# Kernel tuning notes

Hardware: AMD Instinct MI355X
Metric: run time of the kernel (lower is better)

The kernel has to match this reference:

```python
import jax, jax.numpy as jnp
import numpy as np

B, S, H = 1, 2048, 512
E = 16           # num_experts
K = 2            # num_experts_per_tok (norm_topk_prob=False -> no renorm)
I = 4 * H        # routed expert intermediate (mlp_ratio * embed_dim)
IS = 2 * H       # shared expert intermediate (embed_dim * n_shared_experts)


def setup_inputs() -> dict:
    key = jax.random.key(0)
    ks = jax.random.split(key, 9)
    scale = 1.0 / np.sqrt(H)
    return {
        "hidden_states": jax.random.normal(ks[0], (B, S, H), dtype=jnp.float32),
        "gate_w": jax.random.uniform(ks[1], (E, H), jnp.float32, -scale, scale),
        # routed experts, torch Linear weight layout [out, in]
        "w_gate": jax.random.uniform(ks[2], (E, I, H), jnp.float32, -scale, scale),
        "w_up": jax.random.uniform(ks[3], (E, I, H), jnp.float32, -scale, scale),
        "w_down": jax.random.uniform(ks[4], (E, H, I), jnp.float32, -1.0 / np.sqrt(I), 1.0 / np.sqrt(I)),
        # shared expert
        "sw_gate": jax.random.uniform(ks[5], (IS, H), jnp.float32, -scale, scale),
        "sw_up": jax.random.uniform(ks[6], (IS, H), jnp.float32, -scale, scale),
        "sw_down": jax.random.uniform(ks[7], (H, IS), jnp.float32, -1.0 / np.sqrt(IS), 1.0 / np.sqrt(IS)),
    }


def reference(hidden_states, gate_w, w_gate, w_up, w_down, sw_gate, sw_up, sw_down):
    b, s, h = hidden_states.shape
    x = hidden_states.reshape(-1, h)                       # [T, H]
    T = x.shape[0]

    # --- MoEGate: softmax scores, top-k (unnormalized weights) ---
    logits = jnp.einsum("th,eh->te", x, gate_w)            # [T, E]
    scores = jax.nn.softmax(logits, axis=-1)
    topk_w, topk_idx = jax.lax.top_k(scores, K)            # [T, K]

    # combine weights per (token, expert): zero unless selected
    combine = jnp.zeros((T, E), dtype=x.dtype).at[
        jnp.arange(T)[:, None], topk_idx
    ].add(topk_w)                                          # [T, E]

    # --- routed experts (SwiGLU), weighted scatter-combine ---
    g = jnp.einsum("th,eih->tei", x, w_gate)               # [T, E, I]
    u = jnp.einsum("th,eih->tei", x, w_up)
    inter = jax.nn.silu(g) * u                             # [T, E, I]
    y = jnp.einsum("tei,ehi,te->th", inter, w_down, combine)  # [T, H]

    # --- shared expert (always-on SwiGLU) ---
    sg = jax.nn.silu(x @ sw_gate.T) * (x @ sw_up.T)        # [T, IS]
    y = y + sg @ sw_down.T

    return y.reshape(b, s, h)
```

## Files before the change

kernel.cpp:

```cpp
#include <hip/hip_runtime.h>
#include <hip/hip_bf16.h>
#include <math.h>

#define T_TOK 2048
#define H_DIM 512
#define E_NUM 16
#define TOPK  2
#define I_DIM 2048
#define IS_DIM 1024
#define RPMAX 6144
#define NRT128 (RPMAX / 128)
#define NRT64  (RPMAX / 64)

typedef __attribute__((ext_vector_type(8))) short bf16x8;
typedef __attribute__((ext_vector_type(4))) float f32x4;
typedef unsigned short ushort_t;

static __device__ __forceinline__ unsigned short f2bf(float f) {
  unsigned int u = __float_as_uint(f);
  unsigned int r = (u + 0x7fffu + ((u >> 16) & 1u)) >> 16;
  return (unsigned short)r;
}

static __device__ __forceinline__ bf16x8 pack8(float4 a, float4 b) {
  bf16x8 v;
  v[0] = (short)f2bf(a.x); v[1] = (short)f2bf(a.y);
  v[2] = (short)f2bf(a.z); v[3] = (short)f2bf(a.w);
  v[4] = (short)f2bf(b.x); v[5] = (short)f2bf(b.y);
  v[6] = (short)f2bf(b.z); v[7] = (short)f2bf(b.w);
  return v;
}

static __device__ __forceinline__ unsigned long long cvt4(float4 v) {
  __hip_bfloat162 lo = __float22bfloat162_rn(make_float2(v.x, v.y));
  __hip_bfloat162 hi = __float22bfloat162_rn(make_float2(v.z, v.w));
  unsigned int ulo = *(unsigned int*)&lo;
  unsigned int uhi = *(unsigned int*)&hi;
  return ((unsigned long long)uhi << 32) | ulo;
}


template <int LKC>
__global__ __launch_bounds__(256) void gatherA_kernel(const float* __restrict__ x,
                                                      const int* __restrict__ row_token,
                                                      ushort_t* __restrict__ d,
                                                      int n8, int K) {
  const int KC = 1 << LKC;
  int i = blockIdx.x * 256 + threadIdx.x;
  int stride = gridDim.x * 256;
  for (; i < n8; i += stride) {
    int l  = i & 63;
    int fi = i >> 6;
    int kk = fi & (KC - 1);
    int rg = fi >> LKC;
    int row = rg * 16 + (l & 15);
    int tok = row_token ? row_token[row] : row;
    bf16x8 v = {};
    if (tok >= 0) {
      const float* p = x + (size_t)tok * K + kk * 32 + (l >> 4) * 8;
      v = pack8(*(const float4*)p, *(const float4*)(p + 4));
    }
    ((bf16x8*)d)[i] = v;
  }
}

__global__ __launch_bounds__(256) void logits_kernel(
    const float* __restrict__ x, const float* __restrict__ gw,
    float* __restrict__ logits)
{
  __shared__ float xs[16][516];
  int tid = threadIdx.x;
  int t0 = blockIdx.x * 16;
  for (int i = tid; i < 2048; i += 256) {
    int tt = i >> 7, q = i & 127;
    float4 v = ((const float4*)(x + (size_t)(t0 + tt) * H_DIM))[q];
    *(float4*)&xs[tt][q * 4] = v;
  }
  __syncthreads();
  int e = tid >> 4, tt = tid & 15;
  const float* gr = gw + (size_t)e * H_DIM;
  const float* xr = &xs[tt][0];
  int kbase = (blockIdx.x & 7) << 6;
  float acc = 0.f;
  #pragma unroll 8
  for (int kk = 0; kk < H_DIM; kk += 4) {
    int k = (kbase + kk) & (H_DIM - 1);
    float4 b = *(const float4*)(gr + k);
    float4 a = *(const float4*)(xr + k);
    acc += a.x * b.x + a.y * b.y + a.z * b.z + a.w * b.w;
  }
  logits[(size_t)(t0 + tt) * E_NUM + e] = acc;
}

__global__ __launch_bounds__(256) void topk_kernel(
    const float* __restrict__ logits,
    int* __restrict__ topk_idx, float* __restrict__ topk_w, int* __restrict__ counts)
{
  __shared__ int hist[E_NUM];
  int tid = threadIdx.x;
  if (tid < E_NUM) hist[tid] = 0;
  __syncthreads();
  int t = blockIdx.x * 256 + tid;
  float lg[E_NUM];
  #pragma unroll
  for (int i = 0; i < 4; i++) {
    float4 v = ((const float4*)(logits + (size_t)t * E_NUM))[i];
    lg[i * 4] = v.x; lg[i * 4 + 1] = v.y; lg[i * 4 + 2] = v.z; lg[i * 4 + 3] = v.w;
  }
  float mx = lg[0];
  #pragma unroll
  for (int i = 1; i < E_NUM; i++) mx = fmaxf(mx, lg[i]);
  float sc[E_NUM];
  float sum = 0.f;
  #pragma unroll
  for (int i = 0; i < E_NUM; i++) { sc[i] = expf(lg[i] - mx); sum += sc[i]; }
  float inv = 1.f / sum;
  float m1 = -1.f, m2 = -1.f; int i1 = 0, i2 = 0;
  #pragma unroll
  for (int i = 0; i < E_NUM; i++) {
    float s = sc[i] * inv;
    if (s > m1)      { m2 = m1; i2 = i1; m1 = s; i1 = i; }
    else if (s > m2) { m2 = s; i2 = i; }
  }
  topk_idx[t * 2] = i1; topk_idx[t * 2 + 1] = i2;
  topk_w[t * 2] = m1;  topk_w[t * 2 + 1] = m2;
  atomicAdd(&hist[i1], 1);
  atomicAdd(&hist[i2], 1);
  __syncthreads();
  if (tid < E_NUM) atomicAdd(&counts[tid], hist[tid]);
}

__global__ void offsets_kernel(const int* __restrict__ counts,
                               int* __restrict__ offp, int* __restrict__ cursor,
                               int* __restrict__ rt2e, int* __restrict__ rg2e)
{
  __shared__ int offs[E_NUM + 1];
  int tid = threadIdx.x;
  if (tid == 0) {
    int acc = 0;
    #pragma unroll
    for (int e = 0; e < E_NUM; e++) {
      offs[e] = acc; offp[e] = acc;
      acc += (counts[e] + 127) & ~127;
    }
    offs[E_NUM] = acc; offp[E_NUM] = acc;
  }
  if (tid < E_NUM) cursor[tid] = 0;
  __syncthreads();
  for (int r = tid; r < NRT128; r += 128) {
    int row = r << 7; int e = -1;
    #pragma unroll
    for (int i = 0; i < E_NUM; i++)
      if (row >= offs[i] && row < offs[i + 1]) e = i;
    rt2e[r] = e;
  }
  for (int r = tid; r < NRT64; r += 128) {
    int row = r << 6; int e = -1;
    #pragma unroll
    for (int i = 0; i < E_NUM; i++)
      if (row >= offs[i] && row < offs[i + 1]) e = i;
    rg2e[r] = e;
  }
}

__global__ __launch_bounds__(256) void initrows_kernel(int* __restrict__ row_token) {
  int i = blockIdx.x * 256 + threadIdx.x;
  if (i < RPMAX) row_token[i] = -1;
}

__global__ __launch_bounds__(256) void scatter_kernel(
    const int* __restrict__ topk_idx, const float* __restrict__ topk_w,
    const int* __restrict__ offp, int* __restrict__ cursor,
    int* __restrict__ row_token, int* __restrict__ trow)
{
  int t = blockIdx.x * 256 + threadIdx.x;
  if (t >= T_TOK) return;
  #pragma unroll
  for (int k = 0; k < TOPK; k++) {
    int e = topk_idx[t * 2 + k];
    int pos = atomicAdd(&cursor[e], 1);
    int row = offp[e] + pos;
    row_token[row] = t;
    trow[t * 2 + k] = row;
  }
}

__global__ __launch_bounds__(256, 2) void gu12_kernel(
    const ushort_t* __restrict__ xgf, const ushort_t* __restrict__ xsf,
    const float* __restrict__ wg_all, const float* __restrict__ wu_all,
    const float* __restrict__ swg, const float* __restrict__ swu,
    ushort_t* __restrict__ interF, ushort_t* __restrict__ interS,
    const int* __restrict__ rt2e)
{
  const int KC = H_DIM / 32;
  int bid = blockIdx.x;
  int tid = threadIdx.x, w = tid >> 6, l = tid & 63;
  int wm = w >> 1, wn = w & 1;
  int fr = l & 15, g = l >> 4;

  const bf16x8* AF; const float *WG, *WU;
  bf16x8* OP;
  int rg0, c0, kkd0, KCd;

  if (bid < 32 * NRT128) {
    int cb = bid & 31, rt = bid >> 5;
    int e = rt2e[rt]; if (e < 0) return;
    rg0 = rt * 8;
    AF = (const bf16x8*)xgf;
    WG = wg_all + (size_t)e * I_DIM * H_DIM;
    WU = wu_all + (size_t)e * I_DIM * H_DIM;
    c0 = cb * 64;
    KCd = I_DIM >> 5; kkd0 = cb * 2 + wn;
    OP = (bf16x8*)interF;
  } else {
    int b2 = bid - 32 * NRT128;
    int cb = b2 & 15, rt = b2 >> 4;
    rg0 = rt * 8;
    AF = (const bf16x8*)xsf;
    WG = swg; WU = swu;
    c0 = cb * 64;
    KCd = IS_DIM >> 5; kkd0 = cb * 2 + wn;
    OP = (bf16x8*)interS;
  }

  __shared__ ushort_t sm[2][8192];

  const bf16x8* abase[2]; int au[2];
  #pragma unroll
  for (int j = 0; j < 2; j++) {
    int u = tid + j * 256;
    au[j] = u;
    abase[j] = AF + ((size_t)(rg0 + (u >> 6)) * KC) * 64 + (u & 63);
  }
  const float* bgsrc[2]; int bws[2];
  #pragma unroll
  for (int i = 0; i < 2; i++) {
    int f = tid + i * 256;
    int row = f >> 3, q = f & 7;
    bgsrc[i] = WG + (size_t)(c0 + row) * H_DIM + q * 4;
    bws[i] = 8192 + (row >> 4) * 1024 + ((row & 15) + (q >> 1) * 16) * 16 + (q & 1) * 8;
  }
  ptrdiff_t dWU = WU - WG;

  f32x4 accg[4][2] = {}, accu[4][2] = {};
  bf16x8 ra0[2], ra1[2];
  float4 rg0v[2], ru0v[2], rg1v[2], ru1v[2];

  auto loadS0 = [&](int kk) {
    #pragma unroll
    for (int j = 0; j < 2; j++) ra0[j] = abase[j][(size_t)kk * 64];
    #pragma unroll
    for (int i = 0; i < 2; i++) {
      rg0v[i] = *(const float4*)(bgsrc[i] + kk * 32);
      ru0v[i] = *(const float4*)(bgsrc[i] + dWU + kk * 32);
    }
  };
  auto loadS1 = [&](int kk) {
    #pragma unroll
    for (int j = 0; j < 2; j++) ra1[j] = abase[j][(size_t)kk * 64];
    #pragma unroll
    for (int i = 0; i < 2; i++) {
      rg1v[i] = *(const float4*)(bgsrc[i] + kk * 32);
      ru1v[i] = *(const float4*)(bgsrc[i] + dWU + kk * 32);
    }
  };
  auto writeS0 = [&](int b) {
    bf16x8* ap = (bf16x8*)sm[b];
    ap[au[0]] = ra0[0]; ap[au[1]] = ra0[1];
    char* pb = (char*)sm[b];
    #pragma unroll
    for (int i = 0; i < 2; i++) {
      *(unsigned long long*)(pb + bws[i])        = cvt4(rg0v[i]);
      *(unsigned long long*)(pb + bws[i] + 4096) = cvt4(ru0v[i]);
    }
  };
  auto writeS1 = [&](int b) {
    bf16x8* ap = (bf16x8*)sm[b];
    ap[au[0]] = ra1[0]; ap[au[1]] = ra1[1];
    char* pb = (char*)sm[b];
    #pragma unroll
    for (int i = 0; i < 2; i++) {
      *(unsigned long long*)(pb + bws[i])        = cvt4(rg1v[i]);
      *(unsigned long long*)(pb + bws[i] + 4096) = cvt4(ru1v[i]);
    }
  };
  auto compute = [&](int b) {
    char* pb = (char*)sm[b];
    bf16x8 af[4], bg[2], bu[2];
    #pragma unroll
    for (int mi = 0; mi < 4; mi++)
      af[mi] = *(const bf16x8*)(pb + (wm * 4 + mi) * 1024 + l * 16);
    #pragma unroll
    for (int ni = 0; ni < 2; ni++) {
      bg[ni] = *(const bf16x8*)(pb + 8192  + (wn * 2 + ni) * 1024 + l * 16);
      bu[ni] = *(const bf16x8*)(pb + 12288 + (wn * 2 + ni) * 1024 + l * 16);
    }
    __builtin_amdgcn_s_setprio(1);
    #pragma unroll
    for (int mi = 0; mi < 4; mi++)
      #pragma unroll
      for (int ni = 0; ni < 2; ni++) {
        accg[mi][ni] = __builtin_amdgcn_mfma_f32_16x16x32_bf16(af[mi], bg[ni], accg[mi][ni], 0, 0, 0);
        accu[mi][ni] = __builtin_amdgcn_mfma_f32_16x16x32_bf16(af[mi], bu[ni], accu[mi][ni], 0, 0, 0);
      }
    __builtin_amdgcn_s_setprio(0);
  };

  loadS0(0); loadS1(1);
  writeS0(0);
  asm volatile("s_waitcnt lgkmcnt(0)" ::: "memory");
  __builtin_amdgcn_s_barrier();
  for (int kk = 0; kk < KC; kk += 2) {
    if (kk + 2 < KC) loadS0(kk + 2);
    compute(0);
    writeS1(1);
    asm volatile("s_waitcnt lgkmcnt(0)" ::: "memory");
    __builtin_amdgcn_s_barrier();
    if (kk + 3 < KC) loadS1(kk + 3);
    compute(1);
    if (kk + 2 < KC) writeS0(0);
    asm volatile("s_waitcnt lgkmcnt(0)" ::: "memory");
    __builtin_amdgcn_s_barrier();
  }

  ushort_t* bw = &sm[0][0] + w * (64 * 40);
  #pragma unroll
  for (int mi = 0; mi < 4; mi++)
    #pragma unroll
    for (int ni = 0; ni < 2; ni++)
      #pragma unroll
      for (int j = 0; j < 4; j++) {
        float gg = accg[mi][ni][j], uu = accu[mi][ni][j];
        float s = (gg / (1.f + expf(-gg))) * uu;
        bw[(mi * 16 + g * 4 + j) * 40 + ni * 16 + fr] = f2bf(s);
      }
  #pragma unroll
  for (int rgi = 0; rgi < 4; rgi++) {
    bf16x8 v = *(const bf16x8*)&bw[(rgi * 16 + (l & 15)) * 40 + (l >> 4) * 8];
    OP[((size_t)(rg0 + wm * 4 + rgi) * KCd + kkd0) * 64 + l] = v;
  }
}

__global__ __launch_bounds__(256, 2) void down12_kernel(
    const ushort_t* __restrict__ interF, const ushort_t* __restrict__ interS,
    const float* __restrict__ wd_all, const float* __restrict__ swd,
    float* __restrict__ Dr, float* __restrict__ Ds,
    const int* __restrict__ rg2e)
{
  int bid = blockIdx.x;
  int tid = threadIdx.x, w = tid >> 6, l = tid & 63;
  int fr = l & 15, g = l >> 4;

  const bf16x8* AF; const float* WD;
  float* DO;
  int rgA0, c0, nk2, KCa, row0;

  if (bid < 4 * NRT64) {
    int cb = bid & 3, rt = bid >> 2;
    int e = rg2e[rt]; if (e < 0) return;
    AF = (const bf16x8*)interF;
    WD = wd_all + (size_t)e * H_DIM * I_DIM;
    rgA0 = rt * 4; c0 = cb * 128;
    KCa = I_DIM >> 5; nk2 = I_DIM >> 6;
    row0 = rt * 64;
    DO = Dr;
  } else {
    int b2 = bid - 4 * NRT64;
    int cb = b2 & 3, rt = b2 >> 2;
    AF = (const bf16x8*)interS;
    WD = swd;
    rgA0 = rt * 4; c0 = cb * 128;
    KCa = IS_DIM >> 5; nk2 = IS_DIM >> 6;
    row0 = rt * 64;
    DO = Ds;
  }
  int Kd = KCa * 32;

  __shared__ ushort_t sm[2][12288];

  const bf16x8* abase[2]; int au[2];
  #pragma unroll
  for (int j = 0; j < 2; j++) {
    int u = tid + j * 256;
    au[j] = u;
    int ch = u >> 6;
    abase[j] = AF + ((size_t)(rgA0 + (ch >> 1)) * KCa + (ch & 1)) * 64 + (u & 63);
  }
  const float* bsrc[4]; int bws[4];
  #pragma unroll
  for (int i = 0; i < 4; i++) {
    int f = tid + i * 256;
    bsrc[i] = nullptr; bws[i] = 0;
  }
  const float* bsrc8[8]; int bws8[8];
  #pragma unroll
  for (int i = 0; i < 8; i++) {
    int f = tid + i * 256;
    int row = f >> 4, q = f & 15;
    bsrc8[i] = WD + (size_t)(c0 + row) * Kd + q * 4;
    bws8[i] = 8192 + ((row >> 4) * 2 + (q >> 3)) * 1024
            + ((row & 15) + ((q & 7) >> 1) * 16) * 16 + (q & 1) * 8;
  }

  f32x4 acc[4][2] = {};
  bf16x8 ra0[2], ra1[2];
  float4 rb0[8], rb1[8];

  auto loadS0 = [&](int k2) {
    #pragma unroll
    for (int j = 0; j < 2; j++) ra0[j] = abase[j][(size_t)k2 * 128];
    #pragma unroll
    for (int i = 0; i < 8; i++) rb0[i] = *(const float4*)(bsrc8[i] + k2 * 64);
  };
  auto loadS1 = [&](int k2) {
    #pragma unroll
    for (int j = 0; j < 2; j++) ra1[j] = abase[j][(size_t)k2 * 128];
    #pragma unroll
    for (int i = 0; i < 8; i++) rb1[i] = *(const float4*)(bsrc8[i] + k2 * 64);
  };
  auto writeS0 = [&](int b) {
    bf16x8* ap = (bf16x8*)sm[b];
    ap[au[0]] = ra0[0]; ap[au[1]] = ra0[1];
    char* pb = (char*)sm[b];
    #pragma unroll
    for (int i = 0; i < 8; i++)
      *(unsigned long long*)(pb + bws8[i]) = cvt4(rb0[i]);
  };
  auto writeS1 = [&](int b) {
    bf16x8* ap = (bf16x8*)sm[b];
    ap[au[0]] = ra1[0]; ap[au[1]] = ra1[1];
    char* pb = (char*)sm[b];
    #pragma unroll
    for (int i = 0; i < 8; i++)
      *(unsigned long long*)(pb + bws8[i]) = cvt4(rb1[i]);
  };
  auto compute = [&](int b) {
    char* pb = (char*)sm[b];
    __builtin_amdgcn_s_setprio(1);
    #pragma unroll
    for (int s = 0; s < 2; s++) {
      bf16x8 af[4], bf[2];
      #pragma unroll
      for (int mi = 0; mi < 4; mi++)
        af[mi] = *(const bf16x8*)(pb + (mi * 2 + s) * 1024 + l * 16);
      #pragma unroll
      for (int ni = 0; ni < 2; ni++)
        bf[ni] = *(const bf16x8*)(pb + 8192 + ((w * 2 + ni) * 2 + s) * 1024 + l * 16);
      #pragma unroll
      for (int mi = 0; mi < 4; mi++)
        #pragma unroll
        for (int ni = 0; ni < 2; ni++)
          acc[mi][ni] = __builtin_amdgcn_mfma_f32_16x16x32_bf16(af[mi], bf[ni], acc[mi][ni], 0, 0, 0);
    }
    __builtin_amdgcn_s_setprio(0);
  };

  loadS0(0); loadS1(1);
  writeS0(0);
  asm volatile("s_waitcnt lgkmcnt(0)" ::: "memory");
  __builtin_amdgcn_s_barrier();
  for (int k2 = 0; k2 < nk2; k2 += 2) {
    if (k2 + 2 < nk2) loadS0(k2 + 2);
    compute(0);
    writeS1(1);
    asm volatile("s_waitcnt lgkmcnt(0)" ::: "memory");
    __builtin_amdgcn_s_barrier();
    if (k2 + 3 < nk2) loadS1(k2 + 3);
    compute(1);
    if (k2 + 2 < nk2) writeS0(0);
    asm volatile("s_waitcnt lgkmcnt(0)" ::: "memory");
    __builtin_amdgcn_s_barrier();
  }

  #pragma unroll
  for (int mi = 0; mi < 4; mi++)
    #pragma unroll
    for (int ni = 0; ni < 2; ni++)
      #pragma unroll
      for (int j = 0; j < 4; j++)
        DO[(size_t)(row0 + mi * 16 + g * 4 + j) * H_DIM + c0 + w * 32 + ni * 16 + fr]
            = acc[mi][ni][j];
}

__global__ __launch_bounds__(128) void combine_kernel(
    const float* __restrict__ Dr, const float* __restrict__ Ds,
    const int* __restrict__ trow, const float* __restrict__ topk_w,
    float* __restrict__ out)
{
  int t = blockIdx.x, c = threadIdx.x;
  int r0 = trow[t * 2], r1 = trow[t * 2 + 1];
  float w0 = topk_w[t * 2], w1 = topk_w[t * 2 + 1];
  float4 a = ((const float4*)(Dr + (size_t)r0 * H_DIM))[c];
  float4 b = ((const float4*)(Dr + (size_t)r1 * H_DIM))[c];
  float4 s = ((const float4*)(Ds + (size_t)t * H_DIM))[c];
  float4 r;
  r.x = w0 * a.x + w1 * b.x + s.x;
  r.y = w0 * a.y + w1 * b.y + s.y;
  r.z = w0 * a.z + w1 * b.z + s.z;
  r.w = w0 * a.w + w1 * b.w + s.w;
  ((float4*)(out + (size_t)t * H_DIM))[c] = r;
}

extern "C" void kernel_launch(void* const* d_in, const int* in_sizes, int n_in,
                              void* d_out, int out_size, void* d_ws, size_t ws_size,
                              hipStream_t stream) {
  const float* x       = (const float*)d_in[0];
  const float* gate_w  = (const float*)d_in[1];
  const float* w_gate  = (const float*)d_in[2];
  const float* w_up    = (const float*)d_in[3];
  const float* w_down  = (const float*)d_in[4];
  const float* sw_gate = (const float*)d_in[5];
  const float* sw_up   = (const float*)d_in[6];
  const float* sw_down = (const float*)d_in[7];
  float* out = (float*)d_out;

  char* ws = (char*)d_ws;
  int*   counts    = (int*)ws;
  int*   cursor    = (int*)(ws + 64);
  int*   offp      = (int*)(ws + 128);
  int*   rt2e      = (int*)(ws + 256);
  int*   rg2e      = (int*)(ws + 448);
  int*   topk_idx  = (int*)(ws + 832);
  float* topk_w    = (float*)(ws + 17216);
  int*   trow      = (int*)(ws + 33600);
  int*   row_token = (int*)(ws + 49984);
  size_t off = 49984 + (size_t)RPMAX * 4;
  off = (off + 255) & ~(size_t)255;
  float*    logits = (float*)(ws + off);    off += (size_t)T_TOK * E_NUM * 4;
  ushort_t* xgf  = (ushort_t*)(ws + off); off += (size_t)RPMAX * H_DIM * 2;
  ushort_t* xsf  = (ushort_t*)(ws + off); off += (size_t)T_TOK * H_DIM * 2;
  ushort_t* interF = (ushort_t*)(ws + off); off += (size_t)RPMAX * I_DIM * 2;
  ushort_t* interS = (ushort_t*)(ws + off); off += (size_t)T_TOK * IS_DIM * 2;
  float*    Dr     = (float*)(ws + off);    off += (size_t)RPMAX * H_DIM * 4;
  float*    Ds     = (float*)(ws + off);    off += (size_t)T_TOK * H_DIM * 4;

  hipMemsetAsync(counts, 0, 64, stream);
  logits_kernel<<<T_TOK / 16, 256, 0, stream>>>(x, gate_w, logits);
  topk_kernel<<<T_TOK / 256, 256, 0, stream>>>(logits, topk_idx, topk_w, counts);
  offsets_kernel<<<1, 128, 0, stream>>>(counts, offp, cursor, rt2e, rg2e);
  initrows_kernel<<<RPMAX / 256, 256, 0, stream>>>(row_token);
  scatter_kernel<<<(T_TOK + 255) / 256, 256, 0, stream>>>(topk_idx, topk_w, offp, cursor,
                                                          row_token, trow);
  gatherA_kernel<4><<<RPMAX * H_DIM / 8 / 256, 256, 0, stream>>>(
      x, row_token, xgf, RPMAX * H_DIM / 8, H_DIM);
  gatherA_kernel<4><<<T_TOK * H_DIM / 8 / 256, 256, 0, stream>>>(
      x, nullptr, xsf, T_TOK * H_DIM / 8, H_DIM);

  gu12_kernel<<<32 * NRT128 + 16 * 16, 256, 0, stream>>>(
      xgf, xsf, w_gate, w_up, sw_gate, sw_up, interF, interS, rt2e);
  down12_kernel<<<4 * NRT64 + 4 * 32, 256, 0, stream>>>(
      interF, interS, w_down, sw_down, Dr, Ds, rg2e);
  combine_kernel<<<T_TOK, 128, 0, stream>>>(Dr, Ds, trow, topk_w, out);
}
```

Before: 151.5 us.

## Double K-step per stage in gate/up and down GEMMs with 16-byte LDS stores

The gate/up kernel now processes 64 K-elements per pipeline stage (two MFMA K-slices) with a doubled LDS buffer, halving the number of barriers. Both GEMMs change the weight staging so each thread loads eight contiguous fp32 values and writes one 16-byte bf16 vector directly in MFMA fragment layout, replacing 8-byte scattered LDS writes. The down kernel raises its occupancy hint to 3 blocks per CU. The larger LDS footprint in gate/up (64KB per block) may reduce occupancy, and the fp32 weight loads become less coalesced per row.

```diff
diff --git a/kernel.cpp b/kernel.cpp
--- a/kernel.cpp
+++ b/kernel.cpp
@@ -31,12 +31,17 @@
   return v;
 }
 
-static __device__ __forceinline__ unsigned long long cvt4(float4 v) {
-  __hip_bfloat162 lo = __float22bfloat162_rn(make_float2(v.x, v.y));
-  __hip_bfloat162 hi = __float22bfloat162_rn(make_float2(v.z, v.w));
-  unsigned int ulo = *(unsigned int*)&lo;
-  unsigned int uhi = *(unsigned int*)&hi;
-  return ((unsigned long long)uhi << 32) | ulo;
+static __device__ __forceinline__ bf16x8 cvt8(float4 a, float4 b) {
+  __hip_bfloat162 p0 = __float22bfloat162_rn(make_float2(a.x, a.y));
+  __hip_bfloat162 p1 = __float22bfloat162_rn(make_float2(a.z, a.w));
+  __hip_bfloat162 p2 = __float22bfloat162_rn(make_float2(b.x, b.y));
+  __hip_bfloat162 p3 = __float22bfloat162_rn(make_float2(b.z, b.w));
+  union { bf16x8 v; unsigned int u[4]; } r;
+  r.u[0] = *(unsigned int*)&p0;
+  r.u[1] = *(unsigned int*)&p1;
+  r.u[2] = *(unsigned int*)&p2;
+  r.u[3] = *(unsigned int*)&p3;
+  return r.v;
 }
 
 
@@ -185,7 +190,7 @@
   }
 }
 
-__global__ __launch_bounds__(256, 2) void gu12_kernel(
+__global__ __launch_bounds__(256, 2) void gu13_kernel(
     const ushort_t* __restrict__ xgf, const ushort_t* __restrict__ xsf,
     const float* __restrict__ wg_all, const float* __restrict__ wu_all,
     const float* __restrict__ swg, const float* __restrict__ swu,
@@ -193,6 +198,7 @@
     const int* __restrict__ rt2e)
 {
   const int KC = H_DIM / 32;
+  const int NP = KC / 2;
   int bid = blockIdx.x;
   int tid = threadIdx.x, w = tid >> 6, l = tid & 63;
   int wm = w >> 1, wn = w & 1;
@@ -223,104 +229,91 @@
     OP = (bf16x8*)interS;
   }
 
-  __shared__ ushort_t sm[2][8192];
-
-  const bf16x8* abase[2]; int au[2];
-  #pragma unroll
-  for (int j = 0; j < 2; j++) {
+  __shared__ ushort_t sm[2][16384];
+
+  const bf16x8* abase[4]; int auo[4];
+  #pragma unroll
+  for (int j = 0; j < 4; j++) {
     int u = tid + j * 256;
-    au[j] = u;
-    abase[j] = AF + ((size_t)(rg0 + (u >> 6)) * KC) * 64 + (u & 63);
-  }
-  const float* bgsrc[2]; int bws[2];
+    auo[j] = u;
+    int ca = u >> 6, la = u & 63;
+    abase[j] = AF + ((size_t)(rg0 + (ca >> 1)) * KC + (ca & 1)) * 64 + la;
+  }
+  const float* bsrc[2]; int buo[2];
   #pragma unroll
   for (int i = 0; i < 2; i++) {
-    int f = tid + i * 256;
-    int row = f >> 3, q = f & 7;
-    bgsrc[i] = WG + (size_t)(c0 + row) * H_DIM + q * 4;
-    bws[i] = 8192 + (row >> 4) * 1024 + ((row & 15) + (q >> 1) * 16) * 16 + (q & 1) * 8;
+    int u = tid + i * 256;
+    buo[i] = u;
+    int cb2 = u >> 6, lb = u & 63;
+    int row = c0 + (cb2 >> 1) * 16 + (lb & 15);
+    bsrc[i] = WG + (size_t)row * H_DIM + (cb2 & 1) * 32 + (lb >> 4) * 8;
   }
   ptrdiff_t dWU = WU - WG;
 
   f32x4 accg[4][2] = {}, accu[4][2] = {};
-  bf16x8 ra0[2], ra1[2];
-  float4 rg0v[2], ru0v[2], rg1v[2], ru1v[2];
-
-  auto loadS0 = [&](int kk) {
-    #pragma unroll
-    for (int j = 0; j < 2; j++) ra0[j] = abase[j][(size_t)kk * 64];
+  bf16x8 ra[4];
+  float4 rga_[2][2], rua_[2][2];
+
+  auto load = [&](int p) {
+    #pragma unroll
+    for (int j = 0; j < 4; j++) ra[j] = abase[j][(size_t)(2 * p) * 64];
     #pragma unroll
     for (int i = 0; i < 2; i++) {
-      rg0v[i] = *(const float4*)(bgsrc[i] + kk * 32);
-      ru0v[i] = *(const float4*)(bgsrc[i] + dWU + kk * 32);
+      const float* pg = bsrc[i] + p * 64;
+      rga_[i][0] = *(const float4*)pg;
+      rga_[i][1] = *(const float4*)(pg + 4);
+      rua_[i][0] = *(const float4*)(pg + dWU);
+      rua_[i][1] = *(const float4*)(pg + dWU + 4);
     }
   };
-  auto loadS1 = [&](int kk) {
-    #pragma unroll
-    for (int j = 0; j < 2; j++) ra1[j] = abase[j][(size_t)kk * 64];
+  auto store = [&](int b) {
+    char* pb = (char*)sm[b];
+    #pragma unroll
+    for (int j = 0; j < 4; j++)
+      *(bf16x8*)(pb + auo[j] * 16) = ra[j];
     #pragma unroll
     for (int i = 0; i < 2; i++) {
-      rg1v[i] = *(const float4*)(bgsrc[i] + kk * 32);
-      ru1v[i] = *(const float4*)(bgsrc[i] + dWU + kk * 32);
-    }
-  };
-  auto writeS0 = [&](int b) {
-    bf16x8* ap = (bf16x8*)sm[b];
-    ap[au[0]] = ra0[0]; ap[au[1]] = ra0[1];
-    char* pb = (char*)sm[b];
-    #pragma unroll
-    for (int i = 0; i < 2; i++) {
-      *(unsigned long long*)(pb + bws[i])        = cvt4(rg0v[i]);
-      *(unsigned long long*)(pb + bws[i] + 4096) = cvt4(ru0v[i]);
-    }
-  };
-  auto writeS1 = [&](int b) {
-    bf16x8* ap = (bf16x8*)sm[b];
-    ap[au[0]] = ra1[0]; ap[au[1]] = ra1[1];
-    char* pb = (char*)sm[b];
-    #pragma unroll
-    for (int i = 0; i < 2; i++) {
-      *(unsigned long long*)(pb + bws[i])        = cvt4(rg1v[i]);
-      *(unsigned long long*)(pb + bws[i] + 4096) = cvt4(ru1v[i]);
+      *(bf16x8*)(pb + 16384 + buo[i] * 16) = cvt8(rga_[i][0], rga_[i][1]);
+      *(bf16x8*)(pb + 24576 + buo[i] * 16) = cvt8(rua_[i][0], rua_[i][1]);
     }
   };
   auto compute = [&](int b) {
     char* pb = (char*)sm[b];
-    bf16x8 af[4], bg[2], bu[2];
-    #pragma unroll
-    for (int mi = 0; mi < 4; mi++)
-      af[mi] = *(const bf16x8*)(pb + (wm * 4 + mi) * 1024 + l * 16);
-    #pragma unroll
-    for (int ni = 0; ni < 2; ni++) {
-      bg[ni] = *(const bf16x8*)(pb + 8192  + (wn * 2 + ni) * 1024 + l * 16);
-      bu[ni] = *(const bf16x8*)(pb + 12288 + (wn * 2 + ni) * 1024 + l * 16);
-    }
     __builtin_amdgcn_s_setprio(1);
     #pragma unroll
-    for (int mi = 0; mi < 4; mi++)
+    for (int s = 0; s < 2; s++) {
+      bf16x8 af[4], bg[2], bu[2];
+      #pragma unroll
+      for (int mi = 0; mi < 4; mi++)
+        af[mi] = *(const bf16x8*)(pb + ((wm * 4 + mi) * 2 + s) * 1024 + l * 16);
       #pragma unroll
       for (int ni = 0; ni < 2; ni++) {
-        accg[mi][ni] = __builtin_amdgcn_mfma_f32_16x16x32_bf16(af[mi], bg[ni], accg[mi][ni], 0, 0, 0);
-        accu[mi][ni] = __builtin_amdgcn_mfma_f32_16x16x32_bf16(af[mi], bu[ni], accu[mi][ni], 0, 0, 0);
+        bg[ni] = *(const bf16x8*)(pb + 16384 + ((wn * 2 + ni) * 2 + s) * 1024 + l * 16);
+        bu[ni] = *(const bf16x8*)(pb + 24576 + ((wn * 2 + ni) * 2 + s) * 1024 + l * 16);
       }
+      #pragma unroll
+      for (int mi = 0; mi < 4; mi++)
+        #pragma unroll
+        for (int ni = 0; ni < 2; ni++) {
+          accg[mi][ni] = __builtin_amdgcn_mfma_f32_16x16x32_bf16(af[mi], bg[ni], accg[mi][ni], 0, 0, 0);
+          accu[mi][ni] = __builtin_amdgcn_mfma_f32_16x16x32_bf16(af[mi], bu[ni], accu[mi][ni], 0, 0, 0);
+        }
+    }
     __builtin_amdgcn_s_setprio(0);
   };
 
-  loadS0(0); loadS1(1);
-  writeS0(0);
+  load(0);
+  store(0);
   asm volatile("s_waitcnt lgkmcnt(0)" ::: "memory");
   __builtin_amdgcn_s_barrier();
-  for (int kk = 0; kk < KC; kk += 2) {
-    if (kk + 2 < KC) loadS0(kk + 2);
-    compute(0);
-    writeS1(1);
+  int cur = 0;
+  for (int p = 0; p < NP; p++) {
+    if (p + 1 < NP) load(p + 1);
+    compute(cur);
+    if (p + 1 < NP) store(cur ^ 1);
     asm volatile("s_waitcnt lgkmcnt(0)" ::: "memory");
     __builtin_amdgcn_s_barrier();
-    if (kk + 3 < KC) loadS1(kk + 3);
-    compute(1);
-    if (kk + 2 < KC) writeS0(0);
-    asm volatile("s_waitcnt lgkmcnt(0)" ::: "memory");
-    __builtin_amdgcn_s_barrier();
+    cur ^= 1;
   }
 
   ushort_t* bw = &sm[0][0] + w * (64 * 40);
@@ -341,7 +334,7 @@
   }
 }
 
-__global__ __launch_bounds__(256, 2) void down12_kernel(
+__global__ __launch_bounds__(256, 3) void down13_kernel(
     const ushort_t* __restrict__ interF, const ushort_t* __restrict__ interS,
     const float* __restrict__ wd_all, const float* __restrict__ swd,
     float* __restrict__ Dr, float* __restrict__ Ds,
@@ -353,7 +346,7 @@
 
   const bf16x8* AF; const float* WD;
   float* DO;
-  int rgA0, c0, nk2, KCa, row0;
+  int rgA0, c0, NP, KCa, row0;
 
   if (bid < 4 * NRT64) {
     int cb = bid & 3, rt = bid >> 2;
@@ -361,7 +354,7 @@
     AF = (const bf16x8*)interF;
     WD = wd_all + (size_t)e * H_DIM * I_DIM;
     rgA0 = rt * 4; c0 = cb * 128;
-    KCa = I_DIM >> 5; nk2 = I_DIM >> 6;
+    KCa = I_DIM >> 5; NP = I_DIM >> 6;
     row0 = rt * 64;
     DO = Dr;
   } else {
@@ -370,7 +363,7 @@
     AF = (const bf16x8*)interS;
     WD = swd;
     rgA0 = rt * 4; c0 = cb * 128;
-    KCa = IS_DIM >> 5; nk2 = IS_DIM >> 6;
+    KCa = IS_DIM >> 5; NP = IS_DIM >> 6;
     row0 = rt * 64;
     DO = Ds;
   }
@@ -378,61 +371,46 @@
 
   __shared__ ushort_t sm[2][12288];
 
-  const bf16x8* abase[2]; int au[2];
+  const bf16x8* abase[2]; int auo[2];
   #pragma unroll
   for (int j = 0; j < 2; j++) {
     int u = tid + j * 256;
-    au[j] = u;
-    int ch = u >> 6;
-    abase[j] = AF + ((size_t)(rgA0 + (ch >> 1)) * KCa + (ch & 1)) * 64 + (u & 63);
-  }
-  const float* bsrc[4]; int bws[4];
+    auo[j] = u;
+    int ca = u >> 6, la = u & 63;
+    abase[j] = AF + ((size_t)(rgA0 + (ca >> 1)) * KCa + (ca & 1)) * 64 + la;
+  }
+  const float* bsrc[4]; int buo[4];
   #pragma unroll
   for (int i = 0; i < 4; i++) {
-    int f = tid + i * 256;
-    bsrc[i] = nullptr; bws[i] = 0;
-  }
-  const float* bsrc8[8]; int bws8[8];
-  #pragma unroll
-  for (int i = 0; i < 8; i++) {
-    int f = tid + i * 256;
-    int row = f >> 4, q = f & 15;
-    bsrc8[i] = WD + (size_t)(c0 + row) * Kd + q * 4;
-    bws8[i] = 8192 + ((row >> 4) * 2 + (q >> 3)) * 1024
-            + ((row & 15) + ((q & 7) >> 1) * 16) * 16 + (q & 1) * 8;
+    int u = tid + i * 256;
+    buo[i] = u;
+    int cb2 = u >> 6, lb = u & 63;
+    int row = c0 + (cb2 >> 1) * 16 + (lb & 15);
+    bsrc[i] = WD + (size_t)row * Kd + (cb2 & 1) * 32 + (lb >> 4) * 8;
   }
 
   f32x4 acc[4][2] = {};
-  bf16x8 ra0[2], ra1[2];
-  float4 rb0[8], rb1[8];
-
-  auto loadS0 = [&](int k2) {
-    #pragma unroll
-    for (int j = 0; j < 2; j++) ra0[j] = abase[j][(size_t)k2 * 128];
-    #pragma unroll
-    for (int i = 0; i < 8; i++) rb0[i] = *(const float4*)(bsrc8[i] + k2 * 64);
+  bf16x8 ra[2];
+  float4 rb[4][2];
+
+  auto load = [&](int p) {
+    #pragma unroll
+    for (int j = 0; j < 2; j++) ra[j] = abase[j][(size_t)(2 * p) * 64];
+    #pragma unroll
+    for (int i = 0; i < 4; i++) {
+      const float* pg = bsrc[i] + p * 64;
+      rb[i][0] = *(const float4*)pg;
+      rb[i][1] = *(const float4*)(pg + 4);
+    }
   };
-  auto loadS1 = [&](int k2) {
-    #pragma unroll
-    for (int j = 0; j < 2; j++) ra1[j] = abase[j][(size_t)k2 * 128];
-    #pragma unroll
-    for (int i = 0; i < 8; i++) rb1[i] = *(const float4*)(bsrc8[i] + k2 * 64);
-  };
-  auto writeS0 = [&](int b) {
-    bf16x8* ap = (bf16x8*)sm[b];
-    ap[au[0]] = ra0[0]; ap[au[1]] = ra0[1];
+  auto store = [&](int b) {
     char* pb = (char*)sm[b];
     #pragma unroll
-    for (int i = 0; i < 8; i++)
-      *(unsigned long long*)(pb + bws8[i]) = cvt4(rb0[i]);
-  };
-  auto writeS1 = [&](int b) {
-    bf16x8* ap = (bf16x8*)sm[b];
-    ap[au[0]] = ra1[0]; ap[au[1]] = ra1[1];
-    char* pb = (char*)sm[b];
-    #pragma unroll
-    for (int i = 0; i < 8; i++)
-      *(unsigned long long*)(pb + bws8[i]) = cvt4(rb1[i]);
+    for (int j = 0; j < 2; j++)
+      *(bf16x8*)(pb + auo[j] * 16) = ra[j];
+    #pragma unroll
+    for (int i = 0; i < 4; i++)
+      *(bf16x8*)(pb + 8192 + buo[i] * 16) = cvt8(rb[i][0], rb[i][1]);
   };
   auto compute = [&](int b) {
     char* pb = (char*)sm[b];
@@ -455,21 +433,18 @@
     __builtin_amdgcn_s_setprio(0);
   };
 
-  loadS0(0); loadS1(1);
-  writeS0(0);
+  load(0);
+  store(0);
   asm volatile("s_waitcnt lgkmcnt(0)" ::: "memory");
   __builtin_amdgcn_s_barrier();
-  for (int k2 = 0; k2 < nk2; k2 += 2) {
-    if (k2 + 2 < nk2) loadS0(k2 + 2);
-    compute(0);
-    writeS1(1);
+  int cur = 0;
+  for (int p = 0; p < NP; p++) {
+    if (p + 1 < NP) load(p + 1);
+    compute(cur);
+    if (p + 1 < NP) store(cur ^ 1);
     asm volatile("s_waitcnt lgkmcnt(0)" ::: "memory");
     __builtin_amdgcn_s_barrier();
-    if (k2 + 3 < nk2) loadS1(k2 + 3);
-    compute(1);
-    if (k2 + 2 < nk2) writeS0(0);
-    asm volatile("s_waitcnt lgkmcnt(0)" ::: "memory");
-    __builtin_amdgcn_s_barrier();
+    cur ^= 1;
   }
 
   #pragma unroll
@@ -546,9 +521,9 @@
   gatherA_kernel<4><<<T_TOK * H_DIM / 8 / 256, 256, 0, stream>>>(
       x, nullptr, xsf, T_TOK * H_DIM / 8, H_DIM);
 
-  gu12_kernel<<<32 * NRT128 + 16 * 16, 256, 0, stream>>>(
+  gu13_kernel<<<32 * NRT128 + 16 * 16, 256, 0, stream>>>(
       xgf, xsf, w_gate, w_up, sw_gate, sw_up, interF, interS, rt2e);
-  down12_kernel<<<4 * NRT64 + 4 * 32, 256, 0, stream>>>(
+  down13_kernel<<<4 * NRT64 + 4 * 32, 256, 0, stream>>>(
       interF, interS, w_down, sw_down, Dr, Ds, rg2e);
   combine_kernel<<<T_TOK, 128, 0, stream>>>(Dr, Ds, trow, topk_w, out);
 }
```

New measurement: 181.0 us. 1.19x slower.
